# Kernel tuning notes

Hardware: AMD Instinct MI355X
Metric: run time of the kernel (lower is better)

## Reference

```python
import jax, jax.numpy as jnp
import numpy as np

NUM_NODES = 100000
NUM_EDGES = 1600000
IN_DIM = 128
HID = 128
OUT_DIM = 5


def setup_inputs() -> dict:
    key = jax.random.key(0)
    ks = jax.random.split(key, 8)
    x = jax.random.normal(ks[0], (NUM_NODES, IN_DIM), dtype=jnp.float32)
    edges = jax.random.randint(ks[1], (2, NUM_EDGES), 0, NUM_NODES, dtype=jnp.int32)
    s = 1.0 / np.sqrt(IN_DIM)
    W1 = jax.random.uniform(ks[2], (IN_DIM, HID), jnp.float32, -s, s)
    b1 = jax.random.uniform(ks[3], (HID,), jnp.float32, -s, s)
    sh = 1.0 / np.sqrt(HID)
    W2 = jax.random.uniform(ks[4], (HID, HID), jnp.float32, -sh, sh)
    b2 = jax.random.uniform(ks[5], (HID,), jnp.float32, -sh, sh)
    Wp = jax.random.uniform(ks[6], (HID, OUT_DIM), jnp.float32, -sh, sh)
    bp = jax.random.uniform(ks[7], (OUT_DIM,), jnp.float32, -sh, sh)
    return {"x": x, "edges": edges, "W1": W1, "b1": b1, "W2": W2, "b2": b2, "Wp": Wp, "bp": bp}


def _gnn_layer(x, src, tgt, W, b):
    # scatter-add of source features into targets (mean aggregation)
    agg = jax.ops.segment_sum(x[src], tgt, num_segments=NUM_NODES)  # [N, d]
    cnt = jax.ops.segment_sum(jnp.ones_like(tgt, dtype=x.dtype), tgt, num_segments=NUM_NODES)
    cnt = jnp.maximum(cnt, 1.0)  # clamp(min=1)
    agg = agg / cnt[:, None]
    combined = x + agg  # residual
    return jax.nn.relu(combined @ W + b)


def reference(x, edges, W1, b1, W2, b2, Wp, bp):
    src, tgt = edges[0], edges[1]
    h = _gnn_layer(x, src, tgt, W1, b1)
    h = _gnn_layer(h, src, tgt, W2, b2)
    return h @ Wp + bp  # [N, OUT_DIM]
```

## Files before the change

### kernel.cpp

```cpp
#include <hip/hip_runtime.h>

typedef unsigned int uint32;
typedef unsigned short ushort16;

typedef __attribute__((ext_vector_type(8))) short short8;
typedef __attribute__((ext_vector_type(4))) float f32x4;

#define BMAX 512


__device__ __forceinline__ ushort16 f2bf(float f) {
    uint32 u = __float_as_uint(f);
    u += 0x7fffu + ((u >> 16) & 1u);
    return (ushort16)(u >> 16);
}
__device__ __forceinline__ float bfhi(uint32 u) { return __uint_as_float(u & 0xffff0000u); }
__device__ __forceinline__ float bflo(uint32 u) { return __uint_as_float(u << 16); }
__device__ __forceinline__ uint32 pack2(float a, float b) {
    return (uint32)f2bf(a) | ((uint32)f2bf(b) << 16);
}

union U16 { uint4 u; short8 s; };
__device__ __forceinline__ short8 ld_frag(const ushort16* p) {
    U16 x; x.u = *(const uint4*)p; return x.s;
}

#define ACC8(v) \
    acc[0] += bflo(v.x); acc[1] += bfhi(v.x); \
    acc[2] += bflo(v.y); acc[3] += bfhi(v.y); \
    acc[4] += bflo(v.z); acc[5] += bfhi(v.z); \
    acc[6] += bflo(v.w); acc[7] += bfhi(v.w);

__device__ __forceinline__ void bucket_scan(const int* __restrict__ total, int B,
                                            int* bs , int* sd ) {
    int tid = threadIdx.x;
    int v0 = (2 * tid     < B) ? total[2 * tid]     : 0;
    int v1 = (2 * tid + 1 < B) ? total[2 * tid + 1] : 0;
    int s = v0 + v1;
    sd[tid] = s;
    __syncthreads();
    for (int o = 1; o < 256; o <<= 1) {
        int t = (tid >= o) ? sd[tid - o] : 0;
        __syncthreads();
        sd[tid] += t;
        __syncthreads();
    }
    int excl = sd[tid] - s;
    bs[2 * tid]     = excl;
    bs[2 * tid + 1] = excl + v0;
    __syncthreads();
}

__global__ __launch_bounds__(256)
void hist_cvt_prep_kernel(const int* __restrict__ tgt, int* __restrict__ hist,
                          const float* __restrict__ x, uint4* __restrict__ xb,
                          const float* __restrict__ W1, const float* __restrict__ W2,
                          ushort16* __restrict__ Wt1, ushort16* __restrict__ Wt2,
                          int E, int C, int B, int G1, int n64) {
    int tid = threadIdx.x, blk = blockIdx.x;
    if (blk >= G1) {
        const float* W = (blk - G1) ? W2 : W1;
        ushort16* Wt = (blk - G1) ? Wt2 : Wt1;
        for (int i = tid; i < 16384; i += 256) {
            int k = i >> 7, c = i & 127;
            Wt[c * 128 + k] = f2bf(W[i]);
        }
        return;
    }
    __shared__ int lh[BMAX];
    for (int b = tid; b < B; b += 256) lh[b] = 0;
    __syncthreads();
    int e0 = blk * C, e1 = min(e0 + C, E);
    for (int e = e0 + tid; e < e1; e += 256)
        atomicAdd(&lh[tgt[e] >> 8], 1);
    for (int i = blk * 256 + tid; i < n64; i += G1 * 256) {
        const float4* p = (const float4*)x + (size_t)i * 16;
        uint4* q = xb + (size_t)i * 8;
#pragma unroll
        for (int j = 0; j < 8; ++j) {
            float4 a = p[2 * j], bb = p[2 * j + 1];
            uint4 o;
            o.x = pack2(a.x, a.y); o.y = pack2(a.z, a.w);
            o.z = pack2(bb.x, bb.y); o.w = pack2(bb.z, bb.w);
            q[j] = o;
        }
    }
    __syncthreads();
    for (int b = tid; b < B; b += 256) hist[blk * B + b] = lh[b];
}

__global__ __launch_bounds__(256)
void colscan_kernel(int* __restrict__ hist, int* __restrict__ total, int G1, int B) {
    __shared__ int sd[256];
    __shared__ int carrySh;
    int b = blockIdx.x, tid = threadIdx.x;
    if (tid == 0) carrySh = 0;
    __syncthreads();
    for (int g0 = 0; g0 < G1; g0 += 256) {
        int g = g0 + tid;
        int v = (g < G1) ? hist[g * B + b] : 0;
        int c0 = carrySh;
        sd[tid] = v;
        __syncthreads();
        for (int o = 1; o < 256; o <<= 1) {
            int t = (tid >= o) ? sd[tid - o] : 0;
            __syncthreads();
            sd[tid] += t;
            __syncthreads();
        }
        if (g < G1) hist[g * B + b] = sd[tid] - v + c0;
        int tot = sd[255];
        __syncthreads();
        if (tid == 0) carrySh = c0 + tot;
        __syncthreads();
    }
    if (tid == 0) total[b] = carrySh;
}

__global__ __launch_bounds__(256)
void partition_kernel(const int* __restrict__ src, const int* __restrict__ tgt,
                      const int* __restrict__ hist, const int* __restrict__ total,
                      uint32* __restrict__ ebuf, int E, int C, int B) {
    __shared__ int bs[512];
    __shared__ int sd[256];
    __shared__ int cur[BMAX];
    int tid = threadIdx.x, blk = blockIdx.x;
    bucket_scan(total, B, bs, sd);
    for (int b = tid; b < B; b += 256) cur[b] = hist[blk * B + b] + bs[b];
    __syncthreads();
    int e0 = blk * C, e1 = min(e0 + C, E);
    for (int e = e0 + tid; e < e1; e += 256) {
        int t = tgt[e], s = src[e];
        int slot = atomicAdd(&cur[t >> 8], 1);
        ebuf[slot] = ((uint32)(t & 255) << 24) | (uint32)s;
    }
}

__global__ __launch_bounds__(256)
void csr_kernel(const uint32* __restrict__ ebuf, const int* __restrict__ total,
                int* __restrict__ offsets, int* __restrict__ csr, int N, int B, int E) {
    __shared__ int bs[512];
    __shared__ int sd[256];
    __shared__ int cnt[256];
    int b = blockIdx.x, tid = threadIdx.x;
    bucket_scan(total, B, bs, sd);
    int s = bs[b];
    int n = bs[b + 1] - s;
    int t0 = b << 8;
    cnt[tid] = 0;
    __syncthreads();
    for (int i = tid; i < n; i += 256) atomicAdd(&cnt[ebuf[s + i] >> 24], 1);
    __syncthreads();
    int v = cnt[tid];
    sd[tid] = v;
    __syncthreads();
    for (int o = 1; o < 256; o <<= 1) {
        int t = (tid >= o) ? sd[tid - o] : 0;
        __syncthreads();
        sd[tid] += t;
        __syncthreads();
    }
    int excl = sd[tid] - v;
    int t = t0 + tid;
    if (t < N) offsets[t] = s + excl;
    if (b == B - 1 && tid == 255) offsets[N] = E;
    __syncthreads();
    cnt[tid] = s + excl;
    __syncthreads();
    for (int i = tid; i < n; i += 256) {
        uint32 e = ebuf[s + i];
        int slot = atomicAdd(&cnt[e >> 24], 1);
        csr[slot] = (int)(e & 0x00FFFFFFu);
    }
}

__global__ __launch_bounds__(256, 4)
void agg_combine_bf16_kernel(const ushort16* __restrict__ hb,
                             const int* __restrict__ offsets, const int* __restrict__ csr,
                             uint32* __restrict__ outb, int N) {
    int wid = (blockIdx.x * 256 + threadIdx.x) >> 6;
    int lane = threadIdx.x & 63;
    if (wid >= N) return;
    int g = lane >> 4, sl = lane & 15;
    int s0 = offsets[wid];
    int deg = offsets[wid + 1] - s0;
    int fi = sl * 4 + g;
    uint32 su = ((const uint32*)hb)[(size_t)wid * 64 + fi];

    float acc[8];
#pragma unroll
    for (int j = 0; j < 8; ++j) acc[j] = 0.f;

    int base = 0;
    for (; base + 8 <= deg; base += 8) {
        int i0 = csr[s0 + base + g];
        int i1 = csr[s0 + base + 4 + g];
        uint4 v0 = *(const uint4*)(hb + (size_t)i0 * 128 + sl * 8);
        uint4 v1 = *(const uint4*)(hb + (size_t)i1 * 128 + sl * 8);
        ACC8(v0); ACC8(v1);
    }
    for (; base < deg; base += 4) {
        int e = base + g;
        if (e < deg) {
            int s = csr[s0 + e];
            uint4 v = *(const uint4*)(hb + (size_t)s * 128 + sl * 8);
            ACC8(v);
        }
    }
#pragma unroll
    for (int j = 0; j < 8; ++j) {
        acc[j] += __shfl_xor(acc[j], 16, 64);
        acc[j] += __shfl_xor(acc[j], 32, 64);
    }
    float inv = 1.f / fmaxf((float)deg, 1.f);
    float ax = (g == 0) ? acc[0] : (g == 1) ? acc[2] : (g == 2) ? acc[4] : acc[6];
    float ay = (g == 0) ? acc[1] : (g == 1) ? acc[3] : (g == 2) ? acc[5] : acc[7];
    outb[(size_t)wid * 64 + fi] = pack2(bflo(su) + ax * inv, bfhi(su) + ay * inv);
}

__global__ __launch_bounds__(256)
void gemm_mfma_kernel(const ushort16* __restrict__ A, const ushort16* __restrict__ Wt,
                      const float* __restrict__ bias, int M,
                      ushort16* __restrict__ outB,
                      const float* __restrict__ Wp, const float* __restrict__ bp,
                      float* __restrict__ outP) {
    const int tid = threadIdx.x;
    const int lane = tid & 63;
    const int wave = tid >> 6;
    const int l15 = lane & 15;
    const int quad = lane >> 4;
    const int r0 = blockIdx.x * 64 + wave * 16;

    int arow = r0 + l15;
    if (arow >= M) arow = M - 1;
    const ushort16* aptr = A + (size_t)arow * 128 + quad * 8;
    short8 afr[4];
#pragma unroll
    for (int kt = 0; kt < 4; ++kt) afr[kt] = ld_frag(aptr + kt * 32);

    f32x4 acc[8];
#pragma unroll
    for (int t = 0; t < 8; ++t) acc[t] = (f32x4){0.f, 0.f, 0.f, 0.f};

#pragma unroll
    for (int t = 0; t < 8; ++t) {
        const ushort16* bptr = Wt + (size_t)(16 * t + l15) * 128 + quad * 8;
        short8 b0 = ld_frag(bptr);
        short8 b1 = ld_frag(bptr + 32);
        short8 b2 = ld_frag(bptr + 64);
        short8 b3 = ld_frag(bptr + 96);
        acc[t] = __builtin_amdgcn_mfma_f32_16x16x32_bf16(afr[0], b0, acc[t], 0, 0, 0);
        acc[t] = __builtin_amdgcn_mfma_f32_16x16x32_bf16(afr[1], b1, acc[t], 0, 0, 0);
        acc[t] = __builtin_amdgcn_mfma_f32_16x16x32_bf16(afr[2], b2, acc[t], 0, 0, 0);
        acc[t] = __builtin_amdgcn_mfma_f32_16x16x32_bf16(afr[3], b3, acc[t], 0, 0, 0);
    }

    if (outP) {
        float p[4][5];
#pragma unroll
        for (int r = 0; r < 4; ++r)
#pragma unroll
            for (int j = 0; j < 5; ++j) p[r][j] = 0.f;
#pragma unroll
        for (int t = 0; t < 8; ++t) {
            float wpl[5];
#pragma unroll
            for (int j = 0; j < 5; ++j) wpl[j] = Wp[(16 * t + l15) * 5 + j];
            float bt = bias[16 * t + l15];
            float ov[4];
            ov[0] = fmaxf(acc[t].x + bt, 0.f);
            ov[1] = fmaxf(acc[t].y + bt, 0.f);
            ov[2] = fmaxf(acc[t].z + bt, 0.f);
            ov[3] = fmaxf(acc[t].w + bt, 0.f);
#pragma unroll
            for (int r = 0; r < 4; ++r)
#pragma unroll
                for (int j = 0; j < 5; ++j) p[r][j] += ov[r] * wpl[j];
        }
#pragma unroll
        for (int m = 1; m <= 8; m <<= 1)
#pragma unroll
            for (int r = 0; r < 4; ++r)
#pragma unroll
                for (int j = 0; j < 5; ++j) p[r][j] += __shfl_xor(p[r][j], m, 64);
        if (l15 == 0) {
#pragma unroll
            for (int r = 0; r < 4; ++r) {
                int row = r0 + quad * 4 + r;
                if (row < M) {
#pragma unroll
                    for (int j = 0; j < 5; ++j) outP[(size_t)row * 5 + j] = p[r][j] + bp[j];
                }
            }
        }
    } else {
#pragma unroll
        for (int t = 0; t < 8; ++t) {
            float bt = bias[16 * t + l15];
            float ov[4];
            ov[0] = fmaxf(acc[t].x + bt, 0.f);
            ov[1] = fmaxf(acc[t].y + bt, 0.f);
            ov[2] = fmaxf(acc[t].z + bt, 0.f);
            ov[3] = fmaxf(acc[t].w + bt, 0.f);
#pragma unroll
            for (int r = 0; r < 4; ++r) {
                float nb = __shfl_xor(ov[r], 1, 64);
                int row = r0 + quad * 4 + r;
                if (((l15 & 1) == 0) && row < M) {
                    *(uint32*)(outB + (size_t)row * 128 + 16 * t + l15) = pack2(ov[r], nb);
                }
            }
        }
    }
}

extern "C" void kernel_launch(void* const* d_in, const int* in_sizes, int n_in,
                              void* d_out, int out_size, void* d_ws, size_t ws_size,
                              hipStream_t stream) {
    const float* x     = (const float*)d_in[0];
    const int*   edges = (const int*)d_in[1];
    const float* W1    = (const float*)d_in[2];
    const float* b1    = (const float*)d_in[3];
    const float* W2    = (const float*)d_in[4];
    const float* b2    = (const float*)d_in[5];
    const float* Wp    = (const float*)d_in[6];
    const float* bp    = (const float*)d_in[7];
    float* out = (float*)d_out;

    const int N = in_sizes[0] / 128;
    const int E = in_sizes[1] / 2;
    const int* src = edges;
    const int* tgt = edges + E;

    const int B  = (N + 255) >> 8;
    const int C  = 2048;
    const int G1 = (E + C - 1) / C;
    const int n64 = N * 2;

    char* ws = (char*)d_ws;
    size_t off = 0;
    auto alloc = [&](size_t bytes) {
        char* p = ws + off;
        off = (off + bytes + 255) & ~(size_t)255;
        return p;
    };
    int*      offsets = (int*)alloc((size_t)(N + 1) * 4);
    int*      csr     = (int*)alloc((size_t)E * 4);
    ushort16* xb      = (ushort16*)alloc((size_t)N * 128 * 2);
    ushort16* hb1     = (ushort16*)alloc((size_t)N * 128 * 2);
    ushort16* bufAb   = (ushort16*)alloc((size_t)N * 128 * 2);
    ushort16* Wt1     = (ushort16*)alloc(128 * 128 * 2);
    ushort16* Wt2     = (ushort16*)alloc(128 * 128 * 2);
    int*      hist    = (int*)alloc((size_t)G1 * B * 4);
    int*      total   = (int*)alloc((size_t)B * 4);
    uint32*   ebuf    = (uint32*)bufAb;
    (void)ws_size;

    hist_cvt_prep_kernel<<<G1 + 2, 256, 0, stream>>>(tgt, hist, x, (uint4*)xb,
                                                     W1, W2, Wt1, Wt2, E, C, B, G1, n64);
    colscan_kernel<<<B, 256, 0, stream>>>(hist, total, G1, B);
    partition_kernel<<<G1, 256, 0, stream>>>(src, tgt, hist, total, ebuf, E, C, B);
    csr_kernel<<<B, 256, 0, stream>>>(ebuf, total, offsets, csr, N, B, E);

    const int aggBlocks  = (N + 3) / 4;
    const int gemmBlocks = (N + 63) / 64;

    agg_combine_bf16_kernel<<<aggBlocks, 256, 0, stream>>>(xb, offsets, csr, (uint32*)bufAb, N);
    gemm_mfma_kernel<<<gemmBlocks, 256, 0, stream>>>(bufAb, Wt1, b1, N, hb1,
                                                     nullptr, nullptr, nullptr);
    agg_combine_bf16_kernel<<<aggBlocks, 256, 0, stream>>>(hb1, offsets, csr, (uint32*)bufAb, N);
    gemm_mfma_kernel<<<gemmBlocks, 256, 0, stream>>>(bufAb, Wt2, b2, N, nullptr,
                                                     Wp, bp, out);
}
```

Baseline: 380.3 us.

## Store features in node-major 16-column slices and aggregate per slice

Feature buffers are reorganized into 8 slices of 16 bf16 columns, each stored contiguously over all nodes, with the conversion kernel, GEMM A-loads and GEMM output writes adapted to this layout. Aggregation is rewritten so each wave handles one node and one slice, gathering 32-byte segments per neighbor with 8 neighbors in flight per wave. The intent is to shrink the gathered working set per slice to improve cache hit rates for the random neighbor gathers. In exchange, CSR indices are re-read once per slice and each gather touches a smaller fraction of a cache line.

```diff
diff --git a/kernel.cpp b/kernel.cpp
--- a/kernel.cpp
+++ b/kernel.cpp
@@ -24,12 +24,6 @@
 __device__ __forceinline__ short8 ld_frag(const ushort16* p) {
     U16 x; x.u = *(const uint4*)p; return x.s;
 }
-
-#define ACC8(v) \
-    acc[0] += bflo(v.x); acc[1] += bfhi(v.x); \
-    acc[2] += bflo(v.y); acc[3] += bfhi(v.y); \
-    acc[4] += bflo(v.z); acc[5] += bfhi(v.z); \
-    acc[6] += bflo(v.w); acc[7] += bfhi(v.w);
 
 __device__ __forceinline__ void bucket_scan(const int* __restrict__ total, int B,
                                             int* bs , int* sd ) {
@@ -53,10 +47,10 @@
 
 __global__ __launch_bounds__(256)
 void hist_cvt_prep_kernel(const int* __restrict__ tgt, int* __restrict__ hist,
-                          const float* __restrict__ x, uint4* __restrict__ xb,
+                          const float* __restrict__ x, uint4* __restrict__ xbu4,
                           const float* __restrict__ W1, const float* __restrict__ W2,
                           ushort16* __restrict__ Wt1, ushort16* __restrict__ Wt2,
-                          int E, int C, int B, int G1, int n64) {
+                          int E, int C, int B, int G1, int n64, int N) {
     int tid = threadIdx.x, blk = blockIdx.x;
     if (blk >= G1) {
         const float* W = (blk - G1) ? W2 : W1;
@@ -74,15 +68,18 @@
     for (int e = e0 + tid; e < e1; e += 256)
         atomicAdd(&lh[tgt[e] >> 8], 1);
     for (int i = blk * 256 + tid; i < n64; i += G1 * 256) {
-        const float4* p = (const float4*)x + (size_t)i * 16;
-        uint4* q = xb + (size_t)i * 8;
-#pragma unroll
-        for (int j = 0; j < 8; ++j) {
-            float4 a = p[2 * j], bb = p[2 * j + 1];
-            uint4 o;
-            o.x = pack2(a.x, a.y); o.y = pack2(a.z, a.w);
-            o.z = pack2(bb.x, bb.y); o.w = pack2(bb.z, bb.w);
-            q[j] = o;
+        int n = i >> 1, h = i & 1;
+        const float4* p = (const float4*)x + (size_t)n * 32 + h * 16;
+#pragma unroll
+        for (int j = 0; j < 4; ++j) {
+            float4 a = p[4 * j], b = p[4 * j + 1], c = p[4 * j + 2], d = p[4 * j + 3];
+            uint4 o0, o1;
+            o0.x = pack2(a.x, a.y); o0.y = pack2(a.z, a.w);
+            o0.z = pack2(b.x, b.y); o0.w = pack2(b.z, b.w);
+            o1.x = pack2(c.x, c.y); o1.y = pack2(c.z, c.w);
+            o1.z = pack2(d.x, d.y); o1.w = pack2(d.z, d.w);
+            uint4* q = xbu4 + (size_t)(4 * h + j) * N * 2 + (size_t)n * 2;
+            q[0] = o0; q[1] = o1;
         }
     }
     __syncthreads();
@@ -174,48 +171,46 @@
     }
 }
 
-__global__ __launch_bounds__(256, 4)
-void agg_combine_bf16_kernel(const ushort16* __restrict__ hb,
-                             const int* __restrict__ offsets, const int* __restrict__ csr,
-                             uint32* __restrict__ outb, int N) {
-    int wid = (blockIdx.x * 256 + threadIdx.x) >> 6;
+__global__ __launch_bounds__(512)
+void agg_sliced_kernel(const ushort16* __restrict__ xin,
+                       const int* __restrict__ offsets, const int* __restrict__ csr,
+                       ushort16* __restrict__ xout, int N) {
+    int bk = blockIdx.x;
+    int s = bk & 7;
+    int wave = threadIdx.x >> 6;
+    int node = (bk >> 3) * 8 + wave;
+    if (node >= N) return;
     int lane = threadIdx.x & 63;
-    if (wid >= N) return;
-    int g = lane >> 4, sl = lane & 15;
-    int s0 = offsets[wid];
-    int deg = offsets[wid + 1] - s0;
-    int fi = sl * 4 + g;
-    uint32 su = ((const uint32*)hb)[(size_t)wid * 64 + fi];
-
-    float acc[8];
-#pragma unroll
-    for (int j = 0; j < 8; ++j) acc[j] = 0.f;
-
+    int g = lane >> 3, li = lane & 7;
+    const uint32* bin = (const uint32*)(xin + (size_t)s * N * 16);
+    int s0 = offsets[node];
+    int deg = offsets[node + 1] - s0;
+    uint32 su = bin[(size_t)node * 8 + li];
+    float ax = 0.f, ay = 0.f;
     int base = 0;
-    for (; base + 8 <= deg; base += 8) {
+    for (; base + 16 <= deg; base += 16) {
         int i0 = csr[s0 + base + g];
-        int i1 = csr[s0 + base + 4 + g];
-        uint4 v0 = *(const uint4*)(hb + (size_t)i0 * 128 + sl * 8);
-        uint4 v1 = *(const uint4*)(hb + (size_t)i1 * 128 + sl * 8);
-        ACC8(v0); ACC8(v1);
-    }
-    for (; base < deg; base += 4) {
+        int i1 = csr[s0 + base + 8 + g];
+        uint32 v0 = bin[(size_t)i0 * 8 + li];
+        uint32 v1 = bin[(size_t)i1 * 8 + li];
+        ax += bflo(v0); ay += bfhi(v0);
+        ax += bflo(v1); ay += bfhi(v1);
+    }
+    for (; base < deg; base += 8) {
         int e = base + g;
         if (e < deg) {
-            int s = csr[s0 + e];
-            uint4 v = *(const uint4*)(hb + (size_t)s * 128 + sl * 8);
-            ACC8(v);
-        }
-    }
-#pragma unroll
-    for (int j = 0; j < 8; ++j) {
-        acc[j] += __shfl_xor(acc[j], 16, 64);
-        acc[j] += __shfl_xor(acc[j], 32, 64);
-    }
-    float inv = 1.f / fmaxf((float)deg, 1.f);
-    float ax = (g == 0) ? acc[0] : (g == 1) ? acc[2] : (g == 2) ? acc[4] : acc[6];
-    float ay = (g == 0) ? acc[1] : (g == 1) ? acc[3] : (g == 2) ? acc[5] : acc[7];
-    outb[(size_t)wid * 64 + fi] = pack2(bflo(su) + ax * inv, bfhi(su) + ay * inv);
+            uint32 v = bin[(size_t)csr[s0 + e] * 8 + li];
+            ax += bflo(v); ay += bfhi(v);
+        }
+    }
+    ax += __shfl_xor(ax, 8, 64);  ay += __shfl_xor(ay, 8, 64);
+    ax += __shfl_xor(ax, 16, 64); ay += __shfl_xor(ay, 16, 64);
+    ax += __shfl_xor(ax, 32, 64); ay += __shfl_xor(ay, 32, 64);
+    if (g == 0) {
+        float inv = 1.f / fmaxf((float)deg, 1.f);
+        uint32* bout = (uint32*)(xout + (size_t)s * N * 16);
+        bout[(size_t)node * 8 + li] = pack2(bflo(su) + ax * inv, bfhi(su) + ay * inv);
+    }
 }
 
 __global__ __launch_bounds__(256)
@@ -233,10 +228,13 @@
 
     int arow = r0 + l15;
     if (arow >= M) arow = M - 1;
-    const ushort16* aptr = A + (size_t)arow * 128 + quad * 8;
     short8 afr[4];
 #pragma unroll
-    for (int kt = 0; kt < 4; ++kt) afr[kt] = ld_frag(aptr + kt * 32);
+    for (int kt = 0; kt < 4; ++kt) {
+        const ushort16* ap = A + ((size_t)(kt * 2 + (quad >> 1)) * M + arow) * 16
+                               + (quad & 1) * 8;
+        afr[kt] = ld_frag(ap);
+    }
 
     f32x4 acc[8];
 #pragma unroll
@@ -307,7 +305,7 @@
                 float nb = __shfl_xor(ov[r], 1, 64);
                 int row = r0 + quad * 4 + r;
                 if (((l15 & 1) == 0) && row < M) {
-                    *(uint32*)(outB + (size_t)row * 128 + 16 * t + l15) = pack2(ov[r], nb);
+                    *(uint32*)(outB + ((size_t)t * M + row) * 16 + l15) = pack2(ov[r], nb);
                 }
             }
         }
@@ -346,29 +344,29 @@
     };
     int*      offsets = (int*)alloc((size_t)(N + 1) * 4);
     int*      csr     = (int*)alloc((size_t)E * 4);
-    ushort16* xb      = (ushort16*)alloc((size_t)N * 128 * 2);
-    ushort16* hb1     = (ushort16*)alloc((size_t)N * 128 * 2);
-    ushort16* bufAb   = (ushort16*)alloc((size_t)N * 128 * 2);
+    ushort16* xbs     = (ushort16*)alloc((size_t)N * 128 * 2);
+    ushort16* hb1s    = (ushort16*)alloc((size_t)N * 128 * 2);
+    ushort16* combs   = (ushort16*)alloc((size_t)N * 128 * 2);
     ushort16* Wt1     = (ushort16*)alloc(128 * 128 * 2);
     ushort16* Wt2     = (ushort16*)alloc(128 * 128 * 2);
     int*      hist    = (int*)alloc((size_t)G1 * B * 4);
     int*      total   = (int*)alloc((size_t)B * 4);
-    uint32*   ebuf    = (uint32*)bufAb;
+    uint32*   ebuf    = (uint32*)combs;
     (void)ws_size;
 
-    hist_cvt_prep_kernel<<<G1 + 2, 256, 0, stream>>>(tgt, hist, x, (uint4*)xb,
-                                                     W1, W2, Wt1, Wt2, E, C, B, G1, n64);
+    hist_cvt_prep_kernel<<<G1 + 2, 256, 0, stream>>>(tgt, hist, x, (uint4*)xbs,
+                                                     W1, W2, Wt1, Wt2, E, C, B, G1, n64, N);
     colscan_kernel<<<B, 256, 0, stream>>>(hist, total, G1, B);
     partition_kernel<<<G1, 256, 0, stream>>>(src, tgt, hist, total, ebuf, E, C, B);
     csr_kernel<<<B, 256, 0, stream>>>(ebuf, total, offsets, csr, N, B, E);
 
-    const int aggBlocks  = (N + 3) / 4;
+    const int aggBlocks  = ((N + 7) / 8) * 8;
     const int gemmBlocks = (N + 63) / 64;
 
-    agg_combine_bf16_kernel<<<aggBlocks, 256, 0, stream>>>(xb, offsets, csr, (uint32*)bufAb, N);
-    gemm_mfma_kernel<<<gemmBlocks, 256, 0, stream>>>(bufAb, Wt1, b1, N, hb1,
+    agg_sliced_kernel<<<aggBlocks, 512, 0, stream>>>(xbs, offsets, csr, combs, N);
+    gemm_mfma_kernel<<<gemmBlocks, 256, 0, stream>>>(combs, Wt1, b1, N, hb1s,
                                                      nullptr, nullptr, nullptr);
-    agg_combine_bf16_kernel<<<aggBlocks, 256, 0, stream>>>(hb1, offsets, csr, (uint32*)bufAb, N);
-    gemm_mfma_kernel<<<gemmBlocks, 256, 0, stream>>>(bufAb, Wt2, b2, N, nullptr,
+    agg_sliced_kernel<<<aggBlocks, 512, 0, stream>>>(hb1s, offsets, csr, combs, N);
+    gemm_mfma_kernel<<<gemmBlocks, 256, 0, stream>>>(combs, Wt2, b2, N, nullptr,
                                                      Wp, bp, out);
 }
```

Measured after the change: 615.5 us. 1.62x slower.
